# Performance work log

Hardware: AMD Instinct MI355X
Metric: run time of the kernel (lower is better)

Reference implementation:

```python
import jax, jax.numpy as jnp
import numpy as np

B, NK, NQ = 16, 1024, 1024
D_IN, D_V, D_H = 3, 8, 128
NUGGET = 1e-3   # diagonal regularizer for the kriging covariance solve
EPS = 1e-12     # keeps sqrt differentiable at zero distance


def _mlp(x, w1, b1, w2, b2, w3, b3):
    # Linear -> ReLU -> Linear -> ReLU -> Linear (torch Linear: y = x @ W.T + b)
    h = jax.nn.relu(x @ w1.T + b1)
    h = jax.nn.relu(h @ w2.T + b2)
    return h @ w3.T + b3


def _cdist(a, b):
    # a: [B,N,D], b: [B,M,D] -> [B,N,M] Euclidean distances
    d2 = (jnp.sum(a * a, -1)[:, :, None]
          + jnp.sum(b * b, -1)[:, None, :]
          - 2.0 * jnp.einsum('bnd,bmd->bnm', a, b))
    return jnp.sqrt(jnp.maximum(d2, 0.0) + EPS)


def _linear_init(key, out_f, in_f):
    k1, k2 = jax.random.split(key)
    lim = 1.0 / np.sqrt(in_f)
    w = jax.random.uniform(k1, (out_f, in_f), jnp.float32, -lim, lim)
    b = jax.random.uniform(k2, (out_f,), jnp.float32, -lim, lim)
    return w, b


def setup_inputs() -> dict:
    key = jax.random.key(0)
    ks = jax.random.split(key, 10)
    KEY = jax.random.normal(ks[0], (B, NK, D_IN), jnp.float32)
    VALUE = jax.random.normal(ks[1], (B, NK, D_V), jnp.float32)
    QUERY = jax.random.normal(ks[2], (B, NQ, D_IN), jnp.float32)
    W1_w, W1_b = _linear_init(ks[3], D_H, D_IN)
    W2_w, W2_b = _linear_init(ks[4], D_H, D_H)
    W3_w, W3_b = _linear_init(ks[5], D_IN, D_H)
    Wv1_w, Wv1_b = _linear_init(ks[6], D_H, D_V)
    Wv2_w, Wv2_b = _linear_init(ks[7], D_H, D_H)
    Wv3_w, Wv3_b = _linear_init(ks[8], D_V, D_H)
    return dict(KEY=KEY, VALUE=VALUE, QUERY=QUERY,
                W1_w=W1_w, W1_b=W1_b, W2_w=W2_w, W2_b=W2_b, W3_w=W3_w, W3_b=W3_b,
                Wv1_w=Wv1_w, Wv1_b=Wv1_b, Wv2_w=Wv2_w, Wv2_b=Wv2_b, Wv3_w=Wv3_w, Wv3_b=Wv3_b)


def reference(KEY, VALUE, QUERY,
              W1_w, W1_b, W2_w, W2_b, W3_w, W3_b,
              Wv1_w, Wv1_b, Wv2_w, Wv2_b, Wv3_w, Wv3_b):
    # shared MLP on KEY and QUERY, separate MLP on VALUE
    Wk = _mlp(KEY, W1_w, W1_b, W2_w, W2_b, W3_w, W3_b)
    Wq = _mlp(QUERY, W1_w, W1_b, W2_w, W2_b, W3_w, W3_b)
    Wv = _mlp(VALUE, Wv1_w, Wv1_b, Wv2_w, Wv2_b, Wv3_w, Wv3_b)
    VALUE_scale = VALUE * Wv                  # einsum('bij,bij->bij')
    # kriging prediction with learned elementwise coordinate scalings
    Ks = KEY * Wk                             # [B,NK,D_IN]
    Qs = QUERY * Wq                           # [B,NQ,D_IN]
    C_kk = jnp.exp(-_cdist(Ks, Ks)) + NUGGET * jnp.eye(NK, dtype=KEY.dtype)  # [B,NK,NK]
    C_qk = jnp.exp(-_cdist(Qs, Ks))                                          # [B,NQ,NK]
    # kriging weights: solve C_kk @ lam = C_qk^T  -> lam [B,NK,NQ]
    lam = jnp.linalg.solve(C_kk, jnp.swapaxes(C_qk, 1, 2))
    # prediction: weighted sum of scaled values -> [B,NQ,D_V]
    return jnp.einsum('bkq,bkv->bqv', lam, VALUE_scale)
```

## Files before the change

kernel.cpp:

```cpp
#include <hip/hip_runtime.h>
#include <hip/hip_bf16.h>


__device__ __forceinline__ int row_of(int e) {
    int i = (int)((sqrtf(8.0f * (float)e + 1.0f) - 1.0f) * 0.5f);
    while ((i + 1) * (i + 2) / 2 <= e) i++;
    while (i * (i + 1) / 2 > e) i--;
    return i;
}

__global__ void k_transpose(const float* __restrict__ W2, const float* __restrict__ Wv2,
                            float* __restrict__ W2T, float* __restrict__ Wv2T) {
    int tid = blockIdx.x * 256 + threadIdx.x;
    int e = tid & 16383;
    int r = e >> 7, c = e & 127;
    if (tid < 16384) W2T[c * 128 + r] = W2[e];
    else             Wv2T[c * 128 + r] = Wv2[e];
}

template<int DI, int P>
__device__ __forceinline__ void mlp_body(const float* __restrict__ in,
                                         float* __restrict__ out, int base,
                                         const float* __restrict__ W1,
                                         const float* __restrict__ b1,
                                         const float* __restrict__ W2T,
                                         const float* __restrict__ b2,
                                         const float* __restrict__ W3,
                                         const float* __restrict__ b3) {
    __shared__ float xs[P][DI];
    __shared__ float h1[P][128];
    __shared__ float h2[P][129];
    int t = threadIdx.x;
    for (int i = t; i < P * DI; i += 128) xs[i / DI][i % DI] = in[base * DI + i];
    __syncthreads();
    float w1r[DI];
#pragma unroll
    for (int d = 0; d < DI; d++) w1r[d] = W1[t * DI + d];
    float b1t = b1[t], b2t = b2[t];
#pragma unroll
    for (int p = 0; p < P; p++) {
        float s = b1t;
#pragma unroll
        for (int d = 0; d < DI; d++) s += w1r[d] * xs[p][d];
        h1[p][t] = fmaxf(s, 0.0f);
    }
    __syncthreads();
    float acc[P];
#pragma unroll
    for (int p = 0; p < P; p++) acc[p] = b2t;
    for (int k = 0; k < 128; k++) {
        float w = W2T[k * 128 + t];
#pragma unroll
        for (int p = 0; p < P; p++) acc[p] += w * h1[p][k];
    }
#pragma unroll
    for (int p = 0; p < P; p++) h2[p][t] = fmaxf(acc[p], 0.0f);
    __syncthreads();
    if (t < P * DI) {
        int p = t / DI, d = t % DI;
        float s = b3[d];
        for (int k = 0; k < 128; k++) s += W3[d * 128 + k] * h2[p][k];
        int gi = base * DI + t;
        out[gi] = in[gi] * s;
    }
}

__global__ void k_mlp_kq(const float* __restrict__ KEY, float* __restrict__ Ks,
                         const float* __restrict__ QUERY, float* __restrict__ Qs,
                         const float* __restrict__ W1, const float* __restrict__ b1,
                         const float* __restrict__ W2T, const float* __restrict__ b2,
                         const float* __restrict__ W3, const float* __restrict__ b3) {
    if (blockIdx.x < 512)
        mlp_body<3, 32>(KEY, Ks, blockIdx.x * 32, W1, b1, W2T, b2, W3, b3);
    else
        mlp_body<3, 32>(QUERY, Qs, (blockIdx.x - 512) * 32, W1, b1, W2T, b2, W3, b3);
}

__global__ void k_mlp_v(const float* __restrict__ VALUE, float* __restrict__ Vs,
                        const float* __restrict__ W1, const float* __restrict__ b1,
                        const float* __restrict__ W2T, const float* __restrict__ b2,
                        const float* __restrict__ W3, const float* __restrict__ b3) {
    mlp_body<8, 16>(VALUE, Vs, blockIdx.x * 16, W1, b1, W2T, b2, W3, b3);
}

__global__ void k_buildC(const float* __restrict__ Ks, float* __restrict__ C) {
    long idx = (long)blockIdx.x * 256 + threadIdx.x;
    int b = (int)(idx >> 20);
    int rem = (int)(idx & 1048575);
    int i = rem >> 10, j = rem & 1023;
    const float* a = Ks + ((long)b * 1024 + i) * 3;
    const float* bb = Ks + ((long)b * 1024 + j) * 3;
    float d0 = a[0] - bb[0], d1 = a[1] - bb[1], d2 = a[2] - bb[2];
    float dist = sqrtf(d0 * d0 + d1 * d1 + d2 * d2 + 1e-12f);
    float v = __expf(-dist);
    if (i == j) v += 1e-3f;
    C[idx] = v;
}

__device__ __forceinline__ void panel_update(float Treg[4][8], const float (*cv)[8],
                                             const float (*cw)[8], int r0, int c0t) {
#pragma unroll
    for (int h = 0; h < 2; h++) {
        float va4[4][4], wb4[8][4];
#pragma unroll
        for (int i = 0; i < 4; i++) {
            float4 v = *(const float4*)&cv[r0 + i][h * 4];
            va4[i][0] = v.x; va4[i][1] = v.y; va4[i][2] = v.z; va4[i][3] = v.w;
        }
#pragma unroll
        for (int j = 0; j < 8; j++) {
            float4 v = *(const float4*)&cw[c0t + j][h * 4];
            wb4[j][0] = v.x; wb4[j][1] = v.y; wb4[j][2] = v.z; wb4[j][3] = v.w;
        }
#pragma unroll
        for (int i = 0; i < 4; i++)
#pragma unroll
            for (int j = 0; j < 8; j++)
                Treg[i][j] -= va4[i][0] * wb4[j][0] + va4[i][1] * wb4[j][1]
                            + va4[i][2] * wb4[j][2] + va4[i][3] * wb4[j][3];
    }
}

__device__ __forceinline__ void ldl8(int lane, int jb, const float (*Pn)[8],
                                     float (*cv)[8], float (*cw)[8]) {
    int r1 = lane, r2 = 64 + lane;
    float v1[8], v2[8], w1[8], w2[8];
#pragma unroll
    for (int q = 0; q < 8; q++) {
        int j = jb + q;
        int jl = j & 63;
        bool hi = (j >= 64);
        float a1 = Pn[r1][q], a2 = Pn[r2][q];
#pragma unroll
        for (int p = 0; p < 8; p++) {
            if (p < q) {
                float wj = __shfl(hi ? w2[p] : w1[p], jl);
                a1 -= v1[p] * wj;
                a2 -= v2[p] * wj;
            }
        }
        v1[q] = a1; v2[q] = a2;
        float dj = __shfl(hi ? a2 : a1, jl);
        float dinv = 1.0f / dj;
        w1[q] = a1 * dinv; w2[q] = a2 * dinv;
    }
    *(float4*)&cv[r1][0] = make_float4(v1[0], v1[1], v1[2], v1[3]);
    *(float4*)&cv[r1][4] = make_float4(v1[4], v1[5], v1[6], v1[7]);
    *(float4*)&cv[r2][0] = make_float4(v2[0], v2[1], v2[2], v2[3]);
    *(float4*)&cv[r2][4] = make_float4(v2[4], v2[5], v2[6], v2[7]);
    *(float4*)&cw[r1][0] = make_float4(w1[0], w1[1], w1[2], w1[3]);
    *(float4*)&cw[r1][4] = make_float4(w1[4], w1[5], w1[6], w1[7]);
    *(float4*)&cw[r2][0] = make_float4(w2[0], w2[1], w2[2], w2[3]);
    *(float4*)&cw[r2][4] = make_float4(w2[4], w2[5], w2[6], w2[7]);
}

__device__ void potf_body(float* __restrict__ C, float* __restrict__ V,
                          float* smem, int o, int last, int b) {
    int tid = threadIdx.x;
    float* A = C + (long)b * 1048576;
    float* Vp = V + (long)b * 8192;
    float (*T)[132]      = (float(*)[132])smem;
    float (*cv0)[8]      = (float(*)[8])(smem + 16896);
    float (*cw0)[8]      = (float(*)[8])(smem + 17920);
    float (*Pn)[8]       = (float(*)[8])(smem + 18944);
    float (*St)[32][132] = (float(*)[32][132])(smem + 19968);
    float (*Lc)[32][33]  = (float(*)[32][33])(smem + 19968);
    float* rsd           = smem + 28416;
    float (*Wb)[32][33]  = (float(*)[32][33])(smem + 28544);
    float (*zs)[9]       = (float(*)[9])(smem + 30656);
    float (*cv1)[8]      = (float(*)[8])(smem + 31808);
    float (*cw1)[8]      = (float(*)[8])(smem + 32832);

    bool active = (tid < 272);
    int ti = 0, tj = 0, hh = 0;
    if (active) { int e = tid >> 1; hh = tid & 1; ti = row_of(e); tj = e - ti * (ti + 1) / 2; }
    int r0 = ti * 8 + hh * 4, c0t = tj * 8;
    int lane = tid & 63;
    int sr = tid >> 2, slk = (tid & 3) * 8;

    if (o > 0) {
        const float* sp = A + (long)(o + sr) * 1024 + (o - 128) + slk;
        float4 v0 = *(const float4*)sp;
        float4 v1 = *(const float4*)(sp + 4);
        St[0][slk    ][sr] = v0.x; St[0][slk + 1][sr] = v0.y;
        St[0][slk + 2][sr] = v0.z; St[0][slk + 3][sr] = v0.w;
        St[0][slk + 4][sr] = v1.x; St[0][slk + 5][sr] = v1.y;
        St[0][slk + 6][sr] = v1.z; St[0][slk + 7][sr] = v1.w;
    }
    float Treg[4][8];
    if (active) {
        const float* src = A + (long)(o + r0) * 1024 + o + c0t;
#pragma unroll
        for (int i = 0; i < 4; i++) {
            float4 va = *(const float4*)(src + (long)i * 1024);
            float4 vb = *(const float4*)(src + (long)i * 1024 + 4);
            Treg[i][0] = va.x; Treg[i][1] = va.y; Treg[i][2] = va.z; Treg[i][3] = va.w;
            Treg[i][4] = vb.x; Treg[i][5] = vb.y; Treg[i][6] = vb.z; Treg[i][7] = vb.w;
        }
    }
    if (o > 0) {
        for (int kc = 0; kc < 4; kc++) {
            __syncthreads();
            if (kc < 3) {
                const float* sp = A + (long)(o + sr) * 1024 + (o - 128) + (kc + 1) * 32 + slk;
                float4 v0 = *(const float4*)sp;
                float4 v1 = *(const float4*)(sp + 4);
                int nb = (kc + 1) & 1;
                St[nb][slk    ][sr] = v0.x; St[nb][slk + 1][sr] = v0.y;
                St[nb][slk + 2][sr] = v0.z; St[nb][slk + 3][sr] = v0.w;
                St[nb][slk + 4][sr] = v1.x; St[nb][slk + 5][sr] = v1.y;
                St[nb][slk + 6][sr] = v1.z; St[nb][slk + 7][sr] = v1.w;
            }
            if (active) {
                int buf = kc & 1;
#pragma unroll 4
                for (int k = 0; k < 32; k++) {
                    float4 a0 = *(const float4*)&St[buf][k][r0];
                    float4 b0 = *(const float4*)&St[buf][k][c0t];
                    float4 b1 = *(const float4*)&St[buf][k][c0t + 4];
                    float aa[4] = {a0.x, a0.y, a0.z, a0.w};
                    float bb[8] = {b0.x, b0.y, b0.z, b0.w, b1.x, b1.y, b1.z, b1.w};
#pragma unroll
                    for (int i = 0; i < 4; i++)
#pragma unroll
                        for (int j = 0; j < 8; j++) Treg[i][j] -= aa[i] * bb[j];
                }
            }
        }
    }
    if (active && tj == 0) {
#pragma unroll
        for (int i = 0; i < 4; i++) {
            *(float4*)&Pn[r0 + i][0] = make_float4(Treg[i][0], Treg[i][1], Treg[i][2], Treg[i][3]);
            *(float4*)&Pn[r0 + i][4] = make_float4(Treg[i][4], Treg[i][5], Treg[i][6], Treg[i][7]);
        }
    }
    __syncthreads();
    if (tid >= 448) ldl8(tid - 448, 0, Pn, cv0, cw0);
    __syncthreads();
    int cur = 0;
    for (int jbt = 0; jbt < 16; jbt++) {
        float (*cvc)[8] = cur ? cv1 : cv0;
        float (*cwc)[8] = cur ? cw1 : cw0;
        if (active && tj == jbt) {
#pragma unroll
            for (int i = 0; i < 4; i++) {
                float4 va = *(const float4*)&cvc[r0 + i][0];
                float4 vb = *(const float4*)&cvc[r0 + i][4];
                Treg[i][0] = va.x; Treg[i][1] = va.y; Treg[i][2] = va.z; Treg[i][3] = va.w;
                Treg[i][4] = vb.x; Treg[i][5] = vb.y; Treg[i][6] = vb.z; Treg[i][7] = vb.w;
            }
        } else if (active && tj == jbt + 1) {
            panel_update(Treg, cvc, cwc, r0, c0t);
#pragma unroll
            for (int i = 0; i < 4; i++) {
                *(float4*)&Pn[r0 + i][0] = make_float4(Treg[i][0], Treg[i][1], Treg[i][2], Treg[i][3]);
                *(float4*)&Pn[r0 + i][4] = make_float4(Treg[i][4], Treg[i][5], Treg[i][6], Treg[i][7]);
            }
        }
        __syncthreads();
        if (tid >= 448) {
            if (jbt < 15)
                ldl8(tid - 448, (jbt + 1) * 8, Pn, cur ? cv0 : cv1, cur ? cw0 : cw1);
        } else if (active && tj > jbt + 1) {
            panel_update(Treg, cvc, cwc, r0, c0t);
        }
        __syncthreads();
        cur ^= 1;
    }
    if (active) {
#pragma unroll
        for (int i = 0; i < 4; i++) {
            *(float4*)&T[r0 + i][c0t]     = make_float4(Treg[i][0], Treg[i][1], Treg[i][2], Treg[i][3]);
            *(float4*)&T[r0 + i][c0t + 4] = make_float4(Treg[i][4], Treg[i][5], Treg[i][6], Treg[i][7]);
        }
    }
    __syncthreads();
    if (tid < 128) rsd[tid] = rsqrtf(T[tid][tid]);
    __syncthreads();
    {
        int rg = tid >> 5, cg = tid & 31;
#pragma unroll
        for (int j = 0; j < 4; j++) {
            int c = cg + 32 * j;
#pragma unroll
            for (int i = 0; i < 8; i++) {
                int r = rg * 8 + i;
                if (c <= r) T[r][c] *= rsd[c];
                else        T[r][c] = 0.0f;
            }
        }
    }
    __syncthreads();
    {
        int wv = tid >> 6;
        if (wv < 4 && lane < 32) {
            int d0 = wv * 32;
            int j = lane;
            float x[32];
#pragma unroll
            for (int i = 0; i < 32; i++) {
                float dinv = 1.0f / T[d0 + i][d0 + i];
                float s = 0.0f;
#pragma unroll
                for (int k = 0; k < i; k++) s += T[d0 + i][d0 + k] * x[k];
                x[i] = (i == j) ? dinv : -s * dinv;
            }
#pragma unroll
            for (int i = 0; i < 32; i++) T[d0 + i][d0 + j] = x[i];
        }
        if (tid >= 256) {
            for (int idx = tid - 256; idx < 6144; idx += 256) {
                int p = idx >> 10;
                int e = idx & 1023;
                int r = e >> 5, c = e & 31;
                int i3 = (p == 0) ? 1 : (p <= 2 ? 2 : 3);
                int kb = (p == 0) ? 0 : (p <= 2 ? p - 1 : p - 3);
                Lc[p][r][c] = T[i3 * 32 + r][kb * 32 + c];
            }
        }
    }
    __syncthreads();
    {
        int team = tid >> 8, ttid = tid & 255;
        int orr = ttid >> 3, oc = (ttid & 7) * 4;
        for (int st = 0; st < 3; st++) {
            int i3, j3;
            if (team == 0) { i3 = st + 1; j3 = 0; }
            else           { i3 = (st == 0) ? 2 : 3; j3 = (st == 2) ? 2 : 1; }
            float w0 = 0, w1 = 0, w2 = 0, w3 = 0;
            for (int kb = j3; kb < i3; kb++) {
                int p = i3 * (i3 - 1) / 2 + kb;
#pragma unroll 8
                for (int kk = 0; kk < 32; kk++) {
                    float l = Lc[p][orr][kk];
                    w0 += l * T[kb * 32 + kk][j3 * 32 + oc    ];
                    w1 += l * T[kb * 32 + kk][j3 * 32 + oc + 1];
                    w2 += l * T[kb * 32 + kk][j3 * 32 + oc + 2];
                    w3 += l * T[kb * 32 + kk][j3 * 32 + oc + 3];
                }
            }
            Wb[team][orr][oc] = w0; Wb[team][orr][oc + 1] = w1;
            Wb[team][orr][oc + 2] = w2; Wb[team][orr][oc + 3] = w3;
            __syncthreads();
            float v0 = 0, v1 = 0, v2 = 0, v3 = 0;
#pragma unroll 8
            for (int kk = 0; kk < 32; kk++) {
                float l = T[i3 * 32 + orr][i3 * 32 + kk];
                v0 += l * Wb[team][kk][oc    ];
                v1 += l * Wb[team][kk][oc + 1];
                v2 += l * Wb[team][kk][oc + 2];
                v3 += l * Wb[team][kk][oc + 3];
            }
            T[i3 * 32 + orr][j3 * 32 + oc    ] = -v0;
            T[i3 * 32 + orr][j3 * 32 + oc + 1] = -v1;
            T[i3 * 32 + orr][j3 * 32 + oc + 2] = -v2;
            T[i3 * 32 + orr][j3 * 32 + oc + 3] = -v3;
            __syncthreads();
        }
    }
    {
        int r = tid >> 2, c0 = (tid & 3) * 32;
        float* dst = A + (long)(o + r) * 1024 + o + c0;
#pragma unroll
        for (int k = 0; k < 8; k++) {
            int c = c0 + 4 * k;
            *(float4*)(dst + 4 * k) = make_float4(T[r][c], T[r][c + 1], T[r][c + 2], T[r][c + 3]);
        }
    }
    {
        int k = tid >> 2, c2 = (tid & 3) * 2;
        float2 v = *(const float2*)&Vp[(o + k) * 8 + c2];
        zs[k][c2] = v.x; zs[k][c2 + 1] = v.y;
    }
    __syncthreads();
    {
        int r = tid & 127, c2 = (tid >> 7) * 2;
        float y0 = 0, y1 = 0;
#pragma unroll 8
        for (int k = 0; k < 128; k++) {
            float l = T[r][k];
            y0 += l * zs[k][c2];
            y1 += l * zs[k][c2 + 1];
        }
        if (!last) {
            *(float2*)&Vp[(o + r) * 8 + c2] = make_float2(y0, y1);
        } else {
            __syncthreads();
            zs[r][c2] = y0; zs[r][c2 + 1] = y1;
            __syncthreads();
            float x0 = 0, x1 = 0;
#pragma unroll 8
            for (int k = 0; k < 128; k++) {
                float l = T[k][r];
                x0 += l * zs[k][c2];
                x1 += l * zs[k][c2 + 1];
            }
            *(float2*)&Vp[(o + r) * 8 + c2] = make_float2(x0, x1);
        }
    }
}

__device__ void syrk_body(float* __restrict__ C, float* smem,
                          int o, int pti, int ptj, int b) {
    float* A = C + (long)b * 1048576;
    int bi = o + 128 + pti * 128, bj = o + 128 + ptj * 128;
    float (*As)[132] = (float(*)[132])smem;
    float (*Bs)[132] = (float(*)[132])(smem + 4224);
    int tid = threadIdx.x;
    int tx = tid & 15, ty = tid >> 4;
    float acc[4][8] = {};
    int lr = tid >> 2;
    int lk = (tid & 3) * 8;
    bool diag = (bi == bj);
    for (int kc = 0; kc < 128; kc += 32) {
        {
            const float* src = A + (long)(bi + lr) * 1024 + o + kc + lk;
            float4 v0 = *(const float4*)src;
            float4 v1 = *(const float4*)(src + 4);
            As[lk    ][lr] = v0.x; As[lk + 1][lr] = v0.y;
            As[lk + 2][lr] = v0.z; As[lk + 3][lr] = v0.w;
            As[lk + 4][lr] = v1.x; As[lk + 5][lr] = v1.y;
            As[lk + 6][lr] = v1.z; As[lk + 7][lr] = v1.w;
            if (!diag) {
                const float* sb = A + (long)(bj + lr) * 1024 + o + kc + lk;
                float4 w0 = *(const float4*)sb;
                float4 w1 = *(const float4*)(sb + 4);
                Bs[lk    ][lr] = w0.x; Bs[lk + 1][lr] = w0.y;
                Bs[lk + 2][lr] = w0.z; Bs[lk + 3][lr] = w0.w;
                Bs[lk + 4][lr] = w1.x; Bs[lk + 5][lr] = w1.y;
                Bs[lk + 6][lr] = w1.z; Bs[lk + 7][lr] = w1.w;
            }
        }
        __syncthreads();
        {
            float (*Bp)[132] = diag ? As : Bs;
#pragma unroll
            for (int k = 0; k < 32; k++) {
                float4 a0 = *(const float4*)&As[k][ty * 4];
                float4 b0 = *(const float4*)&Bp[k][tx * 8];
                float4 b1 = *(const float4*)&Bp[k][tx * 8 + 4];
                float aa[4] = {a0.x, a0.y, a0.z, a0.w};
                float bb[8] = {b0.x, b0.y, b0.z, b0.w, b1.x, b1.y, b1.z, b1.w};
#pragma unroll
                for (int i = 0; i < 4; i++)
#pragma unroll
                    for (int j = 0; j < 8; j++) acc[i][j] += aa[i] * bb[j];
            }
        }
        __syncthreads();
    }
#pragma unroll
    for (int i = 0; i < 4; i++) {
        int r = bi + ty * 4 + i;
        float* dst = A + (long)r * 1024 + bj + tx * 8;
        if (!diag) {
            float4 p0 = *(const float4*)dst;
            float4 p1 = *(const float4*)(dst + 4);
            p0.x -= acc[i][0]; p0.y -= acc[i][1]; p0.z -= acc[i][2]; p0.w -= acc[i][3];
            p1.x -= acc[i][4]; p1.y -= acc[i][5]; p1.z -= acc[i][6]; p1.w -= acc[i][7];
            *(float4*)dst = p0;
            *(float4*)(dst + 4) = p1;
        } else {
#pragma unroll
            for (int j = 0; j < 8; j++) {
                int c = bj + tx * 8 + j;
                if (c <= r) dst[j] -= acc[i][j];
            }
        }
    }
}

__global__ __launch_bounds__(512) void k_potf_syrk(float* __restrict__ C,
                                                   float* __restrict__ V,
                                                   int o, int last) {
    __shared__ __align__(16) float smem[33856];
    int bx = blockIdx.x;
    if (bx < 16) {
        potf_body(C, V, smem, o, last, bx);
    } else {
        int v = bx - 16;
        int bb = v & 15;
        int p = (v >> 4) + 1;
        int tii = row_of(p);
        int tjj = p - tii * (tii + 1) / 2;
        syrk_body(C, smem, o - 128, tii, tjj, bb);
    }
}

__global__ __launch_bounds__(512) void k_trsmg(float* __restrict__ C,
                                               float* __restrict__ V, int o) {
    int b = blockIdx.y;
    float* A = C + (long)b * 1048576;
    float* Vp = V + (long)b * 8192;
    int bi = o + 128 + blockIdx.x * 128;
    const float* Linv = A + (long)o * 1024 + o;
    __shared__ float As[32][132];
    __shared__ float Ls[32][132];
    int tid = threadIdx.x;
    int tx = tid & 15, ty = tid >> 4;
    float acc[4][8] = {};
    int lr = tid >> 2;
    int lk = (tid & 3) * 8;
    for (int kc = 0; kc < 128; kc += 32) {
        {
            const float* src = A + (long)(bi + lr) * 1024 + o + kc + lk;
            const float* sl  = Linv + (long)lr * 1024 + kc + lk;
            float4 v0 = *(const float4*)src;
            float4 v1 = *(const float4*)(src + 4);
            As[lk    ][lr] = v0.x; As[lk + 1][lr] = v0.y;
            As[lk + 2][lr] = v0.z; As[lk + 3][lr] = v0.w;
            As[lk + 4][lr] = v1.x; As[lk + 5][lr] = v1.y;
            As[lk + 6][lr] = v1.z; As[lk + 7][lr] = v1.w;
            float4 w0 = *(const float4*)sl;
            float4 w1 = *(const float4*)(sl + 4);
            Ls[lk    ][lr] = w0.x; Ls[lk + 1][lr] = w0.y;
            Ls[lk + 2][lr] = w0.z; Ls[lk + 3][lr] = w0.w;
            Ls[lk + 4][lr] = w1.x; Ls[lk + 5][lr] = w1.y;
            Ls[lk + 6][lr] = w1.z; Ls[lk + 7][lr] = w1.w;
        }
        __syncthreads();
#pragma unroll
        for (int k = 0; k < 32; k++) {
            float4 a0 = *(const float4*)&As[k][ty * 4];
            float4 b0 = *(const float4*)&Ls[k][tx * 8];
            float4 b1 = *(const float4*)&Ls[k][tx * 8 + 4];
            float aa[4] = {a0.x, a0.y, a0.z, a0.w};
            float bb[8] = {b0.x, b0.y, b0.z, b0.w, b1.x, b1.y, b1.z, b1.w};
#pragma unroll
            for (int i = 0; i < 4; i++)
#pragma unroll
                for (int j = 0; j < 8; j++) acc[i][j] += aa[i] * bb[j];
        }
        __syncthreads();
    }
#pragma unroll
    for (int i = 0; i < 4; i++) {
        float* dst = A + (long)(bi + ty * 4 + i) * 1024 + o + tx * 8;
        *(float4*)dst       = make_float4(acc[i][0], acc[i][1], acc[i][2], acc[i][3]);
        *(float4*)(dst + 4) = make_float4(acc[i][4], acc[i][5], acc[i][6], acc[i][7]);
    }
    float* ysf = &Ls[0][0];
    {
        int k = tid >> 2, c2 = (tid & 3) * 2;
        float2 v = *(const float2*)&Vp[(o + k) * 8 + c2];
        ysf[k * 9 + c2] = v.x; ysf[k * 9 + c2 + 1] = v.y;
    }
    __syncthreads();
    float zacc0 = 0, zacc1 = 0;
    int zr = tid & 127, zc0 = (tid >> 7) * 2;
#pragma unroll
    for (int ch = 0; ch < 4; ch++) {
        if ((tx >> 2) == ch) {
            int cb = (tx & 3) * 8;
#pragma unroll
            for (int j = 0; j < 8; j++)
#pragma unroll
                for (int i = 0; i < 4; i++)
                    As[cb + j][ty * 4 + i] = acc[i][j];
        }
        __syncthreads();
#pragma unroll 8
        for (int k = 0; k < 32; k++) {
            float l = As[k][zr];
            const float* yp = &ysf[(ch * 32 + k) * 9 + zc0];
            zacc0 += l * yp[0]; zacc1 += l * yp[1];
        }
        __syncthreads();
    }
    float* vp = &Vp[(bi + zr) * 8 + zc0];
    float2 old = *(const float2*)vp;
    old.x -= zacc0; old.y -= zacc1;
    *(float2*)vp = old;
}

__global__ __launch_bounds__(256) void k_bstep(const float* __restrict__ C,
                                               float* __restrict__ V, int k) {
    int b = blockIdx.y, j = blockIdx.x, tid = threadIdx.x;
    const float* A = C + (long)b * 1048576;
    float* Vp = V + (long)b * 8192;
    __shared__ float Lb[128][129];
    __shared__ float xs[128][9];
    __shared__ float ys[128][9];
    {
        int kk = tid >> 1, c0 = (tid & 1) * 4;
        float4 v = *(const float4*)&Vp[(k * 128 + kk) * 8 + c0];
        xs[kk][c0] = v.x; xs[kk][c0+1] = v.y; xs[kk][c0+2] = v.z; xs[kk][c0+3] = v.w;
    }
#pragma unroll
    for (int m = 0; m < 16; m++) {
        int e = tid + m * 256;
        int i = e >> 5, j4 = (e & 31) * 4;
        float4 v = *(const float4*)&A[(long)(k * 128 + i) * 1024 + j * 128 + j4];
        Lb[i][j4] = v.x; Lb[i][j4+1] = v.y; Lb[i][j4+2] = v.z; Lb[i][j4+3] = v.w;
    }
    __syncthreads();
    int r = tid & 127, c0 = (tid >> 7) * 4;
    float u0 = 0, u1 = 0, u2 = 0, u3 = 0;
#pragma unroll 8
    for (int kk = 0; kk < 128; kk++) {
        float l = Lb[kk][r];
        u0 += l * xs[kk][c0    ];
        u1 += l * xs[kk][c0 + 1];
        u2 += l * xs[kk][c0 + 2];
        u3 += l * xs[kk][c0 + 3];
    }
    float* vp = &Vp[(j * 128 + r) * 8 + c0];
    float4 old = *(const float4*)vp;
    old.x -= u0; old.y -= u1; old.z -= u2; old.w -= u3;
    if (j < k - 1) {
        *(float4*)vp = old;
    } else {
        ys[r][c0] = old.x; ys[r][c0+1] = old.y; ys[r][c0+2] = old.z; ys[r][c0+3] = old.w;
        __syncthreads();
        int o = j * 128;
#pragma unroll
        for (int m = 0; m < 16; m++) {
            int e = tid + m * 256;
            int i = e >> 5, j4 = (e & 31) * 4;
            float4 v = *(const float4*)&A[(long)(o + i) * 1024 + o + j4];
            Lb[i][j4] = v.x; Lb[i][j4+1] = v.y; Lb[i][j4+2] = v.z; Lb[i][j4+3] = v.w;
        }
        __syncthreads();
        float x0 = 0, x1 = 0, x2 = 0, x3 = 0;
#pragma unroll 8
        for (int kk = 0; kk < 128; kk++) {
            float l = Lb[kk][r];
            x0 += l * ys[kk][c0    ];
            x1 += l * ys[kk][c0 + 1];
            x2 += l * ys[kk][c0 + 2];
            x3 += l * ys[kk][c0 + 3];
        }
        *(float4*)vp = make_float4(x0, x1, x2, x3);
    }
}

__global__ void k_out(const float* __restrict__ Qs, const float* __restrict__ Ks,
                      const float* __restrict__ X, float* __restrict__ out) {
    int b = blockIdx.x >> 4;
    int qc = blockIdx.x & 15;
    int t = threadIdx.x;
    int q = t & 63, ks = t >> 6;
    __shared__ float kx[1024][3];
    __shared__ __align__(16) float xv[1024][8];
    __shared__ float red[4][64][8];
    for (int i = t; i < 3072; i += 256) kx[i / 3][i % 3] = Ks[b * 3072 + i];
    for (int i = t; i < 8192; i += 256) xv[i >> 3][i & 7] = X[b * 8192 + i];
    __syncthreads();
    int gq = b * 1024 + qc * 64 + q;
    const float* qp = Qs + (long)gq * 3;
    float qx = qp[0], qy = qp[1], qz = qp[2];
    float acc[8] = {};
    int k0 = ks * 256;
#pragma unroll 2
    for (int k = k0; k < k0 + 256; k++) {
        float dx = qx - kx[k][0], dy = qy - kx[k][1], dz = qz - kx[k][2];
        float w = __expf(-sqrtf(dx * dx + dy * dy + dz * dz + 1e-12f));
        float4 xa = *(const float4*)&xv[k][0];
        float4 xb = *(const float4*)&xv[k][4];
        acc[0] += w * xa.x; acc[1] += w * xa.y; acc[2] += w * xa.z; acc[3] += w * xa.w;
        acc[4] += w * xb.x; acc[5] += w * xb.y; acc[6] += w * xb.z; acc[7] += w * xb.w;
    }
#pragma unroll
    for (int c = 0; c < 8; c++) red[ks][q][c] = acc[c];
    __syncthreads();
    if (ks == 0) {
        float* op = out + (long)gq * 8;
#pragma unroll
        for (int c = 0; c < 8; c++)
            op[c] = red[0][q][c] + red[1][q][c] + red[2][q][c] + red[3][q][c];
    }
}

extern "C" void kernel_launch(void* const* d_in, const int* in_sizes, int n_in,
                              void* d_out, int out_size, void* d_ws, size_t ws_size,
                              hipStream_t stream) {
    const float* KEY   = (const float*)d_in[0];
    const float* VALUE = (const float*)d_in[1];
    const float* QUERY = (const float*)d_in[2];
    const float* W1w = (const float*)d_in[3];  const float* W1b = (const float*)d_in[4];
    const float* W2w = (const float*)d_in[5];  const float* W2b = (const float*)d_in[6];
    const float* W3w = (const float*)d_in[7];  const float* W3b = (const float*)d_in[8];
    const float* Wv1w = (const float*)d_in[9]; const float* Wv1b = (const float*)d_in[10];
    const float* Wv2w = (const float*)d_in[11];const float* Wv2b = (const float*)d_in[12];
    const float* Wv3w = (const float*)d_in[13];const float* Wv3b = (const float*)d_in[14];

    float* ws  = (float*)d_ws;
    float* C    = ws;
    float* Ks   = C + 16777216;
    float* Qs   = Ks + 49152;
    float* Vs   = Qs + 49152;
    float* W2T  = Vs + 131072;
    float* Wv2T = W2T + 16384;

    float* out = (float*)d_out;

    hipLaunchKernelGGL(k_transpose, dim3(128), dim3(256), 0, stream, W2w, Wv2w, W2T, Wv2T);
    hipLaunchKernelGGL(k_mlp_kq, dim3(1024), dim3(128), 0, stream,
                       KEY, Ks, QUERY, Qs, W1w, W1b, W2T, W2b, W3w, W3b);
    hipLaunchKernelGGL(k_mlp_v, dim3(1024), dim3(128), 0, stream,
                       VALUE, Vs, Wv1w, Wv1b, Wv2T, Wv2b, Wv3w, Wv3b);
    hipLaunchKernelGGL(k_buildC, dim3(65536), dim3(256), 0, stream, Ks, C);

    for (int s = 0; s < 8; s++) {
        int o = s * 128;
        int np = 0;
        if (s >= 1) { int ntp = 8 - s; np = ntp * (ntp + 1) / 2 - 1; }
        hipLaunchKernelGGL(k_potf_syrk, dim3(16 + np * 16), dim3(512), 0, stream,
                           C, Vs, o, (s == 7) ? 1 : 0);
        int nt = 7 - s;
        if (nt > 0)
            hipLaunchKernelGGL(k_trsmg, dim3(nt, 16), dim3(512), 0, stream, C, Vs, o);
    }
    for (int k = 7; k >= 1; k--)
        hipLaunchKernelGGL(k_bstep, dim3(k, 16), dim3(256), 0, stream, C, Vs, k);

    hipLaunchKernelGGL(k_out, dim3(256), dim3(256), 0, stream, Qs, Ks, Vs, out);
}
```

Measured before the change: 1.071 ms.

## Drop double-buffered LDL lookahead, vectorize triangular-inverse LDS reads, widen back-substitution blocks

The panel LDL factorization no longer runs one step ahead on a dedicated wave with double-buffered cv/cw. Each step now factors the 8-column block on wave 0 and then updates all trailing tiles, using one buffer and shared-memory sync. The triangular-inverse inner loops read T and Wb as float4, and Wb's row pitch goes from 33 to 36 floats for alignment. The back-substitution kernel moves to 512 threads, each handling 2 columns instead of 4. This removes the lookahead overlap, which risks serializing the factorization, but lowers LDS use and may raise occupancy.

```diff
diff --git a/kernel.cpp b/kernel.cpp
--- a/kernel.cpp
+++ b/kernel.cpp
@@ -97,79 +97,20 @@
     C[idx] = v;
 }
 
-__device__ __forceinline__ void panel_update(float Treg[4][8], const float (*cv)[8],
-                                             const float (*cw)[8], int r0, int c0t) {
-#pragma unroll
-    for (int h = 0; h < 2; h++) {
-        float va4[4][4], wb4[8][4];
-#pragma unroll
-        for (int i = 0; i < 4; i++) {
-            float4 v = *(const float4*)&cv[r0 + i][h * 4];
-            va4[i][0] = v.x; va4[i][1] = v.y; va4[i][2] = v.z; va4[i][3] = v.w;
-        }
-#pragma unroll
-        for (int j = 0; j < 8; j++) {
-            float4 v = *(const float4*)&cw[c0t + j][h * 4];
-            wb4[j][0] = v.x; wb4[j][1] = v.y; wb4[j][2] = v.z; wb4[j][3] = v.w;
-        }
-#pragma unroll
-        for (int i = 0; i < 4; i++)
-#pragma unroll
-            for (int j = 0; j < 8; j++)
-                Treg[i][j] -= va4[i][0] * wb4[j][0] + va4[i][1] * wb4[j][1]
-                            + va4[i][2] * wb4[j][2] + va4[i][3] * wb4[j][3];
-    }
-}
-
-__device__ __forceinline__ void ldl8(int lane, int jb, const float (*Pn)[8],
-                                     float (*cv)[8], float (*cw)[8]) {
-    int r1 = lane, r2 = 64 + lane;
-    float v1[8], v2[8], w1[8], w2[8];
-#pragma unroll
-    for (int q = 0; q < 8; q++) {
-        int j = jb + q;
-        int jl = j & 63;
-        bool hi = (j >= 64);
-        float a1 = Pn[r1][q], a2 = Pn[r2][q];
-#pragma unroll
-        for (int p = 0; p < 8; p++) {
-            if (p < q) {
-                float wj = __shfl(hi ? w2[p] : w1[p], jl);
-                a1 -= v1[p] * wj;
-                a2 -= v2[p] * wj;
-            }
-        }
-        v1[q] = a1; v2[q] = a2;
-        float dj = __shfl(hi ? a2 : a1, jl);
-        float dinv = 1.0f / dj;
-        w1[q] = a1 * dinv; w2[q] = a2 * dinv;
-    }
-    *(float4*)&cv[r1][0] = make_float4(v1[0], v1[1], v1[2], v1[3]);
-    *(float4*)&cv[r1][4] = make_float4(v1[4], v1[5], v1[6], v1[7]);
-    *(float4*)&cv[r2][0] = make_float4(v2[0], v2[1], v2[2], v2[3]);
-    *(float4*)&cv[r2][4] = make_float4(v2[4], v2[5], v2[6], v2[7]);
-    *(float4*)&cw[r1][0] = make_float4(w1[0], w1[1], w1[2], w1[3]);
-    *(float4*)&cw[r1][4] = make_float4(w1[4], w1[5], w1[6], w1[7]);
-    *(float4*)&cw[r2][0] = make_float4(w2[0], w2[1], w2[2], w2[3]);
-    *(float4*)&cw[r2][4] = make_float4(w2[4], w2[5], w2[6], w2[7]);
-}
-
 __device__ void potf_body(float* __restrict__ C, float* __restrict__ V,
                           float* smem, int o, int last, int b) {
     int tid = threadIdx.x;
     float* A = C + (long)b * 1048576;
     float* Vp = V + (long)b * 8192;
     float (*T)[132]      = (float(*)[132])smem;
-    float (*cv0)[8]      = (float(*)[8])(smem + 16896);
-    float (*cw0)[8]      = (float(*)[8])(smem + 17920);
+    float (*cv)[8]       = (float(*)[8])(smem + 16896);
+    float (*cw)[8]       = (float(*)[8])(smem + 17920);
     float (*Pn)[8]       = (float(*)[8])(smem + 18944);
     float (*St)[32][132] = (float(*)[32][132])(smem + 19968);
     float (*Lc)[32][33]  = (float(*)[32][33])(smem + 19968);
     float* rsd           = smem + 28416;
-    float (*Wb)[32][33]  = (float(*)[32][33])(smem + 28544);
-    float (*zs)[9]       = (float(*)[9])(smem + 30656);
-    float (*cv1)[8]      = (float(*)[8])(smem + 31808);
-    float (*cw1)[8]      = (float(*)[8])(smem + 32832);
+    float (*Wb)[32][36]  = (float(*)[32][36])(smem + 28544);
+    float (*zs)[9]       = (float(*)[9])(smem + 30848);
 
     bool active = (tid < 272);
     int ti = 0, tj = 0, hh = 0;
@@ -236,37 +177,78 @@
         }
     }
     __syncthreads();
-    if (tid >= 448) ldl8(tid - 448, 0, Pn, cv0, cw0);
-    __syncthreads();
-    int cur = 0;
     for (int jbt = 0; jbt < 16; jbt++) {
-        float (*cvc)[8] = cur ? cv1 : cv0;
-        float (*cwc)[8] = cur ? cw1 : cw0;
+        int jb = jbt * 8;
+        if (tid < 64) {
+            int r1 = lane, r2 = 64 + lane;
+            float v1[8], v2[8], w1[8], w2[8];
+#pragma unroll
+            for (int q = 0; q < 8; q++) {
+                int j = jb + q;
+                int jl = j & 63;
+                bool hi = (j >= 64);
+                float a1 = Pn[r1][q], a2 = Pn[r2][q];
+#pragma unroll
+                for (int p = 0; p < 8; p++) {
+                    if (p < q) {
+                        float wj = __shfl(hi ? w2[p] : w1[p], jl);
+                        a1 -= v1[p] * wj;
+                        a2 -= v2[p] * wj;
+                    }
+                }
+                v1[q] = a1; v2[q] = a2;
+                float dj = __shfl(hi ? a2 : a1, jl);
+                float dinv = 1.0f / dj;
+                w1[q] = a1 * dinv; w2[q] = a2 * dinv;
+            }
+            *(float4*)&cv[r1][0] = make_float4(v1[0], v1[1], v1[2], v1[3]);
+            *(float4*)&cv[r1][4] = make_float4(v1[4], v1[5], v1[6], v1[7]);
+            *(float4*)&cv[r2][0] = make_float4(v2[0], v2[1], v2[2], v2[3]);
+            *(float4*)&cv[r2][4] = make_float4(v2[4], v2[5], v2[6], v2[7]);
+            *(float4*)&cw[r1][0] = make_float4(w1[0], w1[1], w1[2], w1[3]);
+            *(float4*)&cw[r1][4] = make_float4(w1[4], w1[5], w1[6], w1[7]);
+            *(float4*)&cw[r2][0] = make_float4(w2[0], w2[1], w2[2], w2[3]);
+            *(float4*)&cw[r2][4] = make_float4(w2[4], w2[5], w2[6], w2[7]);
+        }
+        __syncthreads();
         if (active && tj == jbt) {
 #pragma unroll
             for (int i = 0; i < 4; i++) {
-                float4 va = *(const float4*)&cvc[r0 + i][0];
-                float4 vb = *(const float4*)&cvc[r0 + i][4];
+                float4 va = *(const float4*)&cv[r0 + i][0];
+                float4 vb = *(const float4*)&cv[r0 + i][4];
                 Treg[i][0] = va.x; Treg[i][1] = va.y; Treg[i][2] = va.z; Treg[i][3] = va.w;
                 Treg[i][4] = vb.x; Treg[i][5] = vb.y; Treg[i][6] = vb.z; Treg[i][7] = vb.w;
             }
-        } else if (active && tj == jbt + 1) {
-            panel_update(Treg, cvc, cwc, r0, c0t);
-#pragma unroll
-            for (int i = 0; i < 4; i++) {
-                *(float4*)&Pn[r0 + i][0] = make_float4(Treg[i][0], Treg[i][1], Treg[i][2], Treg[i][3]);
-                *(float4*)&Pn[r0 + i][4] = make_float4(Treg[i][4], Treg[i][5], Treg[i][6], Treg[i][7]);
-            }
-        }
-        __syncthreads();
-        if (tid >= 448) {
-            if (jbt < 15)
-                ldl8(tid - 448, (jbt + 1) * 8, Pn, cur ? cv0 : cv1, cur ? cw0 : cw1);
-        } else if (active && tj > jbt + 1) {
-            panel_update(Treg, cvc, cwc, r0, c0t);
-        }
-        __syncthreads();
-        cur ^= 1;
+        } else if (active && tj > jbt) {
+#pragma unroll
+            for (int h = 0; h < 2; h++) {
+                float va4[4][4], wb4[8][4];
+#pragma unroll
+                for (int i = 0; i < 4; i++) {
+                    float4 v = *(const float4*)&cv[r0 + i][h * 4];
+                    va4[i][0] = v.x; va4[i][1] = v.y; va4[i][2] = v.z; va4[i][3] = v.w;
+                }
+#pragma unroll
+                for (int j = 0; j < 8; j++) {
+                    float4 v = *(const float4*)&cw[c0t + j][h * 4];
+                    wb4[j][0] = v.x; wb4[j][1] = v.y; wb4[j][2] = v.z; wb4[j][3] = v.w;
+                }
+#pragma unroll
+                for (int i = 0; i < 4; i++)
+#pragma unroll
+                    for (int j = 0; j < 8; j++)
+                        Treg[i][j] -= va4[i][0] * wb4[j][0] + va4[i][1] * wb4[j][1]
+                                    + va4[i][2] * wb4[j][2] + va4[i][3] * wb4[j][3];
+            }
+            if (tj == jbt + 1) {
+#pragma unroll
+                for (int i = 0; i < 4; i++) {
+                    *(float4*)&Pn[r0 + i][0] = make_float4(Treg[i][0], Treg[i][1], Treg[i][2], Treg[i][3]);
+                    *(float4*)&Pn[r0 + i][4] = make_float4(Treg[i][4], Treg[i][5], Treg[i][6], Treg[i][7]);
+                }
+            }
+        }
+        __syncthreads();
     }
     if (active) {
 #pragma unroll
@@ -334,23 +316,18 @@
 #pragma unroll 8
                 for (int kk = 0; kk < 32; kk++) {
                     float l = Lc[p][orr][kk];
-                    w0 += l * T[kb * 32 + kk][j3 * 32 + oc    ];
-                    w1 += l * T[kb * 32 + kk][j3 * 32 + oc + 1];
-                    w2 += l * T[kb * 32 + kk][j3 * 32 + oc + 2];
-                    w3 += l * T[kb * 32 + kk][j3 * 32 + oc + 3];
+                    float4 t = *(const float4*)&T[kb * 32 + kk][j3 * 32 + oc];
+                    w0 += l * t.x; w1 += l * t.y; w2 += l * t.z; w3 += l * t.w;
                 }
             }
-            Wb[team][orr][oc] = w0; Wb[team][orr][oc + 1] = w1;
-            Wb[team][orr][oc + 2] = w2; Wb[team][orr][oc + 3] = w3;
+            *(float4*)&Wb[team][orr][oc] = make_float4(w0, w1, w2, w3);
             __syncthreads();
             float v0 = 0, v1 = 0, v2 = 0, v3 = 0;
 #pragma unroll 8
             for (int kk = 0; kk < 32; kk++) {
                 float l = T[i3 * 32 + orr][i3 * 32 + kk];
-                v0 += l * Wb[team][kk][oc    ];
-                v1 += l * Wb[team][kk][oc + 1];
-                v2 += l * Wb[team][kk][oc + 2];
-                v3 += l * Wb[team][kk][oc + 3];
+                float4 wv = *(const float4*)&Wb[team][kk][oc];
+                v0 += l * wv.x; v1 += l * wv.y; v2 += l * wv.z; v3 += l * wv.w;
             }
             T[i3 * 32 + orr][j3 * 32 + oc    ] = -v0;
             T[i3 * 32 + orr][j3 * 32 + oc + 1] = -v1;
@@ -474,7 +451,7 @@
 __global__ __launch_bounds__(512) void k_potf_syrk(float* __restrict__ C,
                                                    float* __restrict__ V,
                                                    int o, int last) {
-    __shared__ __align__(16) float smem[33856];
+    __shared__ __align__(16) float smem[32000];
     int bx = blockIdx.x;
     if (bx < 16) {
         potf_body(C, V, smem, o, last, bx);
@@ -574,7 +551,7 @@
     *(float2*)vp = old;
 }
 
-__global__ __launch_bounds__(256) void k_bstep(const float* __restrict__ C,
+__global__ __launch_bounds__(512) void k_bstep(const float* __restrict__ C,
                                                float* __restrict__ V, int k) {
     int b = blockIdx.y, j = blockIdx.x, tid = threadIdx.x;
     const float* A = C + (long)b * 1048576;
@@ -583,55 +560,51 @@
     __shared__ float xs[128][9];
     __shared__ float ys[128][9];
     {
-        int kk = tid >> 1, c0 = (tid & 1) * 4;
-        float4 v = *(const float4*)&Vp[(k * 128 + kk) * 8 + c0];
-        xs[kk][c0] = v.x; xs[kk][c0+1] = v.y; xs[kk][c0+2] = v.z; xs[kk][c0+3] = v.w;
-    }
-#pragma unroll
-    for (int m = 0; m < 16; m++) {
-        int e = tid + m * 256;
+        int kk = tid >> 2, c2 = (tid & 3) * 2;
+        float2 v = *(const float2*)&Vp[(k * 128 + kk) * 8 + c2];
+        xs[kk][c2] = v.x; xs[kk][c2 + 1] = v.y;
+    }
+#pragma unroll
+    for (int m = 0; m < 8; m++) {
+        int e = tid + m * 512;
         int i = e >> 5, j4 = (e & 31) * 4;
         float4 v = *(const float4*)&A[(long)(k * 128 + i) * 1024 + j * 128 + j4];
         Lb[i][j4] = v.x; Lb[i][j4+1] = v.y; Lb[i][j4+2] = v.z; Lb[i][j4+3] = v.w;
     }
     __syncthreads();
-    int r = tid & 127, c0 = (tid >> 7) * 4;
-    float u0 = 0, u1 = 0, u2 = 0, u3 = 0;
+    int r = tid & 127, c2 = (tid >> 7) * 2;
+    float u0 = 0, u1 = 0;
 #pragma unroll 8
     for (int kk = 0; kk < 128; kk++) {
         float l = Lb[kk][r];
-        u0 += l * xs[kk][c0    ];
-        u1 += l * xs[kk][c0 + 1];
-        u2 += l * xs[kk][c0 + 2];
-        u3 += l * xs[kk][c0 + 3];
-    }
-    float* vp = &Vp[(j * 128 + r) * 8 + c0];
-    float4 old = *(const float4*)vp;
-    old.x -= u0; old.y -= u1; old.z -= u2; old.w -= u3;
+        u0 += l * xs[kk][c2];
+        u1 += l * xs[kk][c2 + 1];
+    }
+    float* vp = &Vp[(j * 128 + r) * 8 + c2];
+    float2 old = *(const float2*)vp;
+    old.x -= u0; old.y -= u1;
     if (j < k - 1) {
-        *(float4*)vp = old;
+        *(float2*)vp = old;
     } else {
-        ys[r][c0] = old.x; ys[r][c0+1] = old.y; ys[r][c0+2] = old.z; ys[r][c0+3] = old.w;
+        ys[r][c2] = old.x; ys[r][c2 + 1] = old.y;
         __syncthreads();
         int o = j * 128;
 #pragma unroll
-        for (int m = 0; m < 16; m++) {
-            int e = tid + m * 256;
+        for (int m = 0; m < 8; m++) {
+            int e = tid + m * 512;
             int i = e >> 5, j4 = (e & 31) * 4;
             float4 v = *(const float4*)&A[(long)(o + i) * 1024 + o + j4];
             Lb[i][j4] = v.x; Lb[i][j4+1] = v.y; Lb[i][j4+2] = v.z; Lb[i][j4+3] = v.w;
         }
         __syncthreads();
-        float x0 = 0, x1 = 0, x2 = 0, x3 = 0;
+        float x0 = 0, x1 = 0;
 #pragma unroll 8
         for (int kk = 0; kk < 128; kk++) {
             float l = Lb[kk][r];
-            x0 += l * ys[kk][c0    ];
-            x1 += l * ys[kk][c0 + 1];
-            x2 += l * ys[kk][c0 + 2];
-            x3 += l * ys[kk][c0 + 3];
-        }
-        *(float4*)vp = make_float4(x0, x1, x2, x3);
+            x0 += l * ys[kk][c2];
+            x1 += l * ys[kk][c2 + 1];
+        }
+        *(float2*)vp = make_float2(x0, x1);
     }
 }
 
@@ -713,7 +686,7 @@
             hipLaunchKernelGGL(k_trsmg, dim3(nt, 16), dim3(512), 0, stream, C, Vs, o);
     }
     for (int k = 7; k >= 1; k--)
-        hipLaunchKernelGGL(k_bstep, dim3(k, 16), dim3(256), 0, stream, C, Vs, k);
+        hipLaunchKernelGGL(k_bstep, dim3(k, 16), dim3(512), 0, stream, C, Vs, k);
 
     hipLaunchKernelGGL(k_out, dim3(256), dim3(256), 0, stream, Qs, Ks, Vs, out);
 }
```

Result: faster. 973.0 us (-9.2%).
